# Kernel tuning notes

Hardware: AMD Instinct MI355X
Metric: run time of the kernel (lower is better)

The kernel has to match this reference:

```python
import jax, jax.numpy as jnp
import numpy as np
import math

B, H, W, C = 8, 112, 112, 192
WS, SHIFT, NH = 7, 3, 6
HD = C // NH
N = WS * WS
NW = (H // WS) * (W // WS)
MLP_HID = 4 * C
LOG100 = math.log(100.0)


def _rel_table():
    ch = np.arange(-(WS - 1), WS, dtype=np.float32)
    t = np.stack(np.meshgrid(ch, ch, indexing='ij')).transpose(1, 2, 0).reshape(-1, 2)
    t = t / float(WS - 1) * 8.0
    t = np.sign(t) * np.log2(np.abs(t) + 1.0) / np.log2(8.0)
    return t.astype(np.float32)  # ((2*WS-1)^2, 2)


def _rel_index():
    coords = np.stack(np.meshgrid(np.arange(WS), np.arange(WS), indexing='ij')).reshape(2, -1)
    rel = (coords[:, :, None] - coords[:, None, :]).transpose(1, 2, 0)
    rel = rel + np.array([WS - 1, WS - 1])
    rel = rel * np.array([2 * WS - 1, 1])
    return rel.sum(-1).astype(np.int32)  # (N, N)


def _attn_mask():
    img = np.zeros((H, W), dtype=np.float32)
    cnt = 0
    for hsl in (slice(0, -WS), slice(-WS, -SHIFT), slice(-SHIFT, None)):
        for wsl in (slice(0, -WS), slice(-WS, -SHIFT), slice(-SHIFT, None)):
            img[hsl, wsl] = cnt
            cnt += 1
    mw = img.reshape(H // WS, WS, W // WS, WS).transpose(0, 2, 1, 3).reshape(-1, N)
    diff = mw[:, None, :] - mw[:, :, None]
    return np.where(diff != 0, -100.0, 0.0).astype(np.float32)  # (NW, N, N)

REL_TABLE = jnp.asarray(_rel_table())
REL_INDEX = jnp.asarray(_rel_index())
ATTN_MASK = jnp.asarray(_attn_mask())


def _ln(v, g, b, eps=1e-5):
    m = jnp.mean(v, axis=-1, keepdims=True)
    s = jnp.mean((v - m) ** 2, axis=-1, keepdims=True)
    return (v - m) / jnp.sqrt(s + eps) * g + b


def setup_inputs() -> dict:
    key = jax.random.key(0)
    ks = jax.random.split(key, 12)
    std = 0.02
    inp = {
        'x': jax.random.normal(ks[0], (B, H * W, C), jnp.float32),
        'q_w': jax.random.normal(ks[1], (C, C), jnp.float32) * std,
        'q_b': jnp.zeros((C,), jnp.float32),
        'k_w': jax.random.normal(ks[2], (C, C), jnp.float32) * std,
        'v_w': jax.random.normal(ks[3], (C, C), jnp.float32) * std,
        'v_b': jnp.zeros((C,), jnp.float32),
        'proj_w': jax.random.normal(ks[4], (C, C), jnp.float32) * std,
        'proj_b': jnp.zeros((C,), jnp.float32),
        'logit_scale': jnp.log(10.0 * jnp.ones((NH, 1, 1), jnp.float32)),
        'cpb_w0': jax.random.normal(ks[5], (2, 512), jnp.float32) * std,
        'cpb_b0': jnp.zeros((512,), jnp.float32),
        'cpb_w1': jax.random.normal(ks[6], (512, NH), jnp.float32) * std,
        'ln1_g': jnp.ones((C,), jnp.float32),
        'ln1_b': jnp.zeros((C,), jnp.float32),
        'ln2_g': jnp.ones((C,), jnp.float32),
        'ln2_b': jnp.zeros((C,), jnp.float32),
        'fc1_w': jax.random.normal(ks[7], (C, MLP_HID), jnp.float32) * std,
        'fc1_b': jnp.zeros((MLP_HID,), jnp.float32),
        'fc2_w': jax.random.normal(ks[8], (MLP_HID, C), jnp.float32) * std,
        'fc2_b': jnp.zeros((C,), jnp.float32),
    }
    return inp


def reference(x, q_w, q_b, k_w, v_w, v_b, proj_w, proj_b, logit_scale,
              cpb_w0, cpb_b0, cpb_w1, ln1_g, ln1_b, ln2_g, ln2_b,
              fc1_w, fc1_b, fc2_w, fc2_b):
    shortcut = x  # (B, L, C)
    h = x.reshape(B, H, W, C)
    # cyclic shift
    h = jnp.roll(h, shift=(-SHIFT, -SHIFT), axis=(1, 2))
    # window partition -> (B*NW, N, C)
    h = h.reshape(B, H // WS, WS, W // WS, WS, C).transpose(0, 1, 3, 2, 4, 5)
    h = h.reshape(B * NW, N, C)

    q = (h @ q_w + q_b).reshape(-1, N, NH, HD).transpose(0, 2, 1, 3)
    k = (h @ k_w).reshape(-1, N, NH, HD).transpose(0, 2, 1, 3)
    v = (h @ v_w + v_b).reshape(-1, N, NH, HD).transpose(0, 2, 1, 3)

    # cosine-similarity attention
    q = q / jnp.maximum(jnp.linalg.norm(q, axis=-1, keepdims=True), 1e-6)
    k = k / jnp.maximum(jnp.linalg.norm(k, axis=-1, keepdims=True), 1e-6)
    scale = jnp.exp(jnp.minimum(logit_scale, LOG100))  # (NH,1,1)
    attn = jnp.einsum('bhqd,bhkd->bhqk', q, k) * scale

    # relative position bias via CPB MLP
    rpb = jax.nn.relu(REL_TABLE @ cpb_w0 + cpb_b0) @ cpb_w1  # (169, NH)
    rpb = rpb[REL_INDEX.reshape(-1)].reshape(N, N, NH).transpose(2, 0, 1)
    rpb = 16.0 * jax.nn.sigmoid(rpb)  # (NH, N, N)
    attn = attn + rpb[None]

    # shift mask
    attn = attn.reshape(B, NW, NH, N, N) + ATTN_MASK[None, :, None]
    attn = attn.reshape(B * NW, NH, N, N)
    attn = jax.nn.softmax(attn, axis=-1)

    out = jnp.einsum('bhqk,bhkd->bhqd', attn, v)
    out = out.transpose(0, 2, 1, 3).reshape(B * NW, N, C)
    out = out @ proj_w + proj_b

    # window reverse + reverse shift
    out = out.reshape(B, H // WS, W // WS, WS, WS, C).transpose(0, 1, 3, 2, 4, 5)
    out = out.reshape(B, H, W, C)
    out = jnp.roll(out, shift=(SHIFT, SHIFT), axis=(1, 2)).reshape(B, H * W, C)

    # post-norm residual (Swin-v2)
    h1 = shortcut + _ln(out, ln1_g, ln1_b)
    mlp = jax.nn.gelu(h1 @ fc1_w + fc1_b) @ fc2_w + fc2_b
    return h1 + _ln(mlp, ln2_g, ln2_b)
```

## Files before the change

### kernel.cpp

```cpp
#include <hip/hip_runtime.h>

typedef unsigned short u16;
typedef unsigned int   u32;
typedef __attribute__((ext_vector_type(8))) short bf16x8;
typedef __attribute__((ext_vector_type(4))) float f32x4;

#define B_      8
#define HW_     112
#define C_      192
#define NH_     6
#define HD_     32
#define L_      (HW_*HW_)
#define M_      (B_*L_)
#define MLP_    768
#define QKVN_   576
#define LOG100_ 4.6051702f
#define LOG2E_  1.44269504f

__device__ __forceinline__ float bf2f(u16 u){
  union { float f; u32 i; } v; v.i = ((u32)u) << 16; return v.f;
}
__device__ __forceinline__ u16 f2bf(float f){
  union { float f; u32 i; } v; v.f = f;
  u32 r = (v.i + 0x7fffu + ((v.i >> 16) & 1u)) >> 16;
  return (u16)r;
}
__device__ __forceinline__ u32 pk2(float a, float b){
  return (u32)f2bf(a) | ((u32)f2bf(b) << 16);
}
__device__ __forceinline__ u32 cvtpk(float a, float b){
  u32 r;
  asm volatile("v_cvt_pk_bf16_f32 %0, %1, %2" : "=v"(r) : "v"(a), "v"(b));
  return r;
}
__device__ __forceinline__ void u4_to_f8(uint4 u, float* f){
  f[0]=bf2f((u16)(u.x&0xffffu)); f[1]=bf2f((u16)(u.x>>16));
  f[2]=bf2f((u16)(u.y&0xffffu)); f[3]=bf2f((u16)(u.y>>16));
  f[4]=bf2f((u16)(u.z&0xffffu)); f[5]=bf2f((u16)(u.z>>16));
  f[6]=bf2f((u16)(u.w&0xffffu)); f[7]=bf2f((u16)(u.w>>16));
}

__device__ __forceinline__ int rowelem(int b, int wh, int ww, int t){
  int i = t/7, j = t - i*7;
  int oi = wh*7 + i + 3; if (oi >= 112) oi -= 112;
  int oj = ww*7 + j + 3; if (oj >= 112) oj -= 112;
  return b*L_ + oi*112 + oj;
}

__global__ __launch_bounds__(256) void prep_weights(
    const float* __restrict__ qw, const float* __restrict__ qb,
    const float* __restrict__ kw, const float* __restrict__ vw,
    const float* __restrict__ vb, const float* __restrict__ pw,
    const float* __restrict__ pb, const float* __restrict__ f1w,
    const float* __restrict__ f1b, const float* __restrict__ f2w,
    const float* __restrict__ f2b,
    u16* __restrict__ wt_qkv, float* __restrict__ b_qkv,
    u16* __restrict__ wt_p,   float* __restrict__ b_p,
    u16* __restrict__ wt_f1,  float* __restrict__ b_f1,
    u16* __restrict__ wt_f2,  float* __restrict__ b_f2)
{
  const int S1 = 110592, S2 = 147456, S3 = 294912, S4 = 442368, TOT = 444096;
  int i = blockIdx.x*256 + threadIdx.x;
  if (i >= TOT) return;
  if (i < S1) {
    int n = i/192, k = i%192;
    float v = (n<192) ? qw[k*192+n] : ((n<384) ? kw[k*192+(n-192)] : vw[k*192+(n-384)]);
    wt_qkv[i] = f2bf(v);
  } else if (i < S2) {
    int j = i - S1; int n = j/192, k = j%192;
    wt_p[j] = f2bf(pw[k*192+n]);
  } else if (i < S3) {
    int j = i - S2; int n = j/192, k = j%192;
    wt_f1[j] = f2bf(f1w[k*768+n]);
  } else if (i < S4) {
    int j = i - S3; int n = j/768, k = j%768;
    wt_f2[j] = f2bf(f2w[k*192+n]);
  } else {
    int j = i - S4;
    if (j < 576)        b_qkv[j] = (j<192) ? qb[j] : ((j<384) ? 0.f : vb[j-384]);
    else if (j < 768)   b_p[j-576]   = pb[j-576];
    else if (j < 1536)  b_f1[j-768]  = f1b[j-768];
    else                b_f2[j-1536] = f2b[j-1536];
  }
}

__device__ __forceinline__ float reltab(float x){
  float v = x * (8.f/6.f);
  float r = __log2f(fabsf(v) + 1.f) * (1.f/3.f);
  return (v < 0.f) ? -r : r;
}

__global__ __launch_bounds__(64) void rpb_a_kernel(
    const float* __restrict__ w0, const float* __restrict__ b0,
    const float* __restrict__ w1, float* __restrict__ rpb169)
{
  int tt = blockIdx.x, lane = threadIdx.x;
  float t0 = reltab((float)(tt/13 - 6));
  float t1 = reltab((float)(tt%13 - 6));
  float acc[6] = {0.f,0.f,0.f,0.f,0.f,0.f};
  for (int j = lane; j < 512; j += 64){
    float hid = fmaxf(t0*w0[j] + t1*w0[512+j] + b0[j], 0.f);
#pragma unroll
    for (int h=0; h<6; h++) acc[h] += hid * w1[j*6+h];
  }
#pragma unroll
  for (int h=0; h<6; h++){
#pragma unroll
    for (int m=32; m>=1; m>>=1) acc[h] += __shfl_xor(acc[h], m);
  }
  if (lane == 0){
#pragma unroll
    for (int h=0; h<6; h++) rpb169[tt*6+h] = acc[h];
  }
}

__global__ __launch_bounds__(256) void rpb_b_kernel(
    const float* __restrict__ rpb169, float* __restrict__ biasQ)
{
  int i = blockIdx.x*256 + threadIdx.x;
  if (i >= 98304) return;
  int key = i & 63, q = (i >> 6) & 63;
  int rest = i >> 12;
  int hh = rest % 6, type = rest / 6;
  float val;
  if (key >= 49) val = -60000.f;
  else if (q >= 49) val = 0.f;
  else {
    int qi = q/7, qj = q%7, ki = key/7, kj = key%7;
    int idx = (qi - ki + 6)*13 + (qj - kj + 6);
    float x = rpb169[idx*6 + hh];
    float sig = 16.f / (1.f + __expf(-x));
    int th = type >> 1, tw = type & 1;
    int rq = (th ? (qi<4?1:2) : 0)*3 + (tw ? (qj<4?1:2) : 0);
    int rk = (th ? (ki<4?1:2) : 0)*3 + (tw ? (kj<4?1:2) : 0);
    float msk = (rq != rk) ? -100.f : 0.f;
    val = (sig + msk) * LOG2E_;
  }
  biasQ[i] = val;
}

__device__ __forceinline__ float fast_gelu(float v){
  float t = v*v;
  float w = v * fmaf(-0.1029432f, t, -2.30220817f);
  float e = exp2f(w);
  return v * __builtin_amdgcn_rcpf(1.f + e);
}

template<int K, bool GELU>
__global__ __launch_bounds__(512,4) void gemm_kernel(
    const u16* __restrict__ A, const u16* __restrict__ Wt,
    const float* __restrict__ bias, u16* __restrict__ out, int NN)
{
  __shared__ __align__(16) u16 lds[10240];
  const int tid  = threadIdx.x;
  const int wave = tid >> 6, lane = tid & 63;
  const int m0 = blockIdx.x * 128;
  const int n0 = blockIdx.y * 192;
  const int wr = wave >> 1, wc = wave & 1;
  const int lrow = lane >> 2, lslot = lane & 3;
  const int gk = (lslot ^ ((lrow >> 1) & 3)) * 8;

  const u16* gsrc[3]; u32 ldst[3]; int nst = (wave < 4) ? 3 : 2;
#pragma unroll
  for (int t=0; t<3; t++){
    int c = wave + t*8;
    if (c < 8)       { gsrc[t] = A  + (size_t)(m0 + c*16 + lrow)*K + gk;      ldst[t] = c*512; }
    else if (c < 20) { gsrc[t] = Wt + (size_t)(n0 + (c-8)*16 + lrow)*K + gk;  ldst[t] = 4096 + (c-8)*512; }
  }
  const int lr16 = lane & 15;
  const int slot8 = ((lane >> 4) ^ ((lr16 >> 1) & 3)) * 8;
  u32 aoff[2], boff[6];
#pragma unroll
  for (int mt=0; mt<2; mt++) aoff[mt] = (u32)((wr*32 + mt*16 + lr16)*32 + slot8);
#pragma unroll
  for (int nt=0; nt<6; nt++) boff[nt] = (u32)(4096 + (wc*96 + nt*16 + lr16)*32 + slot8);

  float bs[6];
#pragma unroll
  for (int nt=0; nt<6; nt++) bs[nt] = bias[n0 + wc*96 + nt*16 + lr16];

  f32x4 acc[2][6];
#pragma unroll
  for (int mt=0; mt<2; mt++)
#pragma unroll
    for (int nt=0; nt<6; nt++)
      acc[mt][nt] = (f32x4){0.f,0.f,0.f,0.f};

  for (int k0 = 0; k0 < K; k0 += 32) {
#pragma unroll
    for (int t=0; t<3; t++){
      if (t < nst) {
        __builtin_amdgcn_global_load_lds(
            (const __attribute__((address_space(1))) void*)gsrc[t],
            (__attribute__((address_space(3))) void*)&lds[ldst[t]], 16, 0, 0);
        gsrc[t] += 32;
      }
    }
    __syncthreads();
    bf16x8 af[2], bf[6];
#pragma unroll
    for (int mt=0; mt<2; mt++) af[mt] = *(const bf16x8*)&lds[aoff[mt]];
#pragma unroll
    for (int nt=0; nt<6; nt++) bf[nt] = *(const bf16x8*)&lds[boff[nt]];
#pragma unroll
    for (int mt=0; mt<2; mt++)
#pragma unroll
      for (int nt=0; nt<6; nt++)
        acc[mt][nt] = __builtin_amdgcn_mfma_f32_16x16x32_bf16(af[mt], bf[nt], acc[mt][nt], 0, 0, 0);
    __syncthreads();
  }
#pragma unroll
  for (int mt=0; mt<2; mt++){
    int rbase = m0 + wr*32 + mt*16 + (lane >> 4)*4;
#pragma unroll
    for (int nt=0; nt<6; nt++){
      int col = n0 + wc*96 + nt*16 + lr16;
#pragma unroll
      for (int r2=0; r2<4; r2++){
        float v = acc[mt][nt][r2] + bs[nt];
        if (GELU) v = fast_gelu(v);
        out[(size_t)(rbase + r2)*NN + col] = f2bf(v);
      }
    }
  }
}

__global__ __launch_bounds__(512,4) void gemm_qkv_kernel(
    const float* __restrict__ X, const u16* __restrict__ Wt,
    const float* __restrict__ bias, u16* __restrict__ out)
{
  __shared__ __align__(16) u16 lds[10240];
  const int tid  = threadIdx.x;
  const int wave = tid >> 6, lane = tid & 63;
  const int m0 = blockIdx.x * 128;
  const int n0 = blockIdx.y * 192;
  const int wr = wave >> 1, wc = wave & 1;
  const int lrow = lane >> 2, lslot = lane & 3;
  const int gk = (lslot ^ ((lrow >> 1) & 3)) * 8;

  const u16* gsrcB[2]; u32 ldstB[2]; int nstB = (wave < 4) ? 2 : 1;
#pragma unroll
  for (int t=0; t<2; t++){
    int c = wave + t*8;
    if (c < 12) { gsrcB[t] = Wt + (size_t)(n0 + c*16 + lrow)*192 + gk; ldstB[t] = 4096 + c*512; }
  }
  const int ar = tid >> 2, as = tid & 3;
  const float* gsrcA = X + (size_t)(m0 + ar)*192 + as*8;
  const u32 dsta = (u32)(ar*32 + (as ^ ((ar >> 1) & 3))*8);

  const int lr16 = lane & 15;
  const int slot8 = ((lane >> 4) ^ ((lr16 >> 1) & 3)) * 8;
  u32 aoff[2], boff[6];
#pragma unroll
  for (int mt=0; mt<2; mt++) aoff[mt] = (u32)((wr*32 + mt*16 + lr16)*32 + slot8);
#pragma unroll
  for (int nt=0; nt<6; nt++) boff[nt] = (u32)(4096 + (wc*96 + nt*16 + lr16)*32 + slot8);

  float bs[6];
#pragma unroll
  for (int nt=0; nt<6; nt++) bs[nt] = bias[n0 + wc*96 + nt*16 + lr16];

  f32x4 acc[2][6];
#pragma unroll
  for (int mt=0; mt<2; mt++)
#pragma unroll
    for (int nt=0; nt<6; nt++)
      acc[mt][nt] = (f32x4){0.f,0.f,0.f,0.f};

  for (int k0 = 0; k0 < 192; k0 += 32) {
#pragma unroll
    for (int t=0; t<2; t++){
      if (t < nstB) {
        __builtin_amdgcn_global_load_lds(
            (const __attribute__((address_space(1))) void*)gsrcB[t],
            (__attribute__((address_space(3))) void*)&lds[ldstB[t]], 16, 0, 0);
        gsrcB[t] += 32;
      }
    }
    float4 a0 = *(const float4*)gsrcA;
    float4 a1 = *(const float4*)(gsrcA + 4);
    gsrcA += 32;
    uint4 aw;
    aw.x = cvtpk(a0.y, a0.x); aw.x = pk2(a0.x, a0.y);
    aw.x = pk2(a0.x, a0.y); aw.y = pk2(a0.z, a0.w);
    aw.z = pk2(a1.x, a1.y); aw.w = pk2(a1.z, a1.w);
    *(uint4*)(void*)&lds[dsta] = aw;
    __syncthreads();
    bf16x8 af[2], bf[6];
#pragma unroll
    for (int mt=0; mt<2; mt++) af[mt] = *(const bf16x8*)&lds[aoff[mt]];
#pragma unroll
    for (int nt=0; nt<6; nt++) bf[nt] = *(const bf16x8*)&lds[boff[nt]];
#pragma unroll
    for (int mt=0; mt<2; mt++)
#pragma unroll
      for (int nt=0; nt<6; nt++)
        acc[mt][nt] = __builtin_amdgcn_mfma_f32_16x16x32_bf16(af[mt], bf[nt], acc[mt][nt], 0, 0, 0);
    __syncthreads();
  }
#pragma unroll
  for (int mt=0; mt<2; mt++){
    int rbase = m0 + wr*32 + mt*16 + (lane >> 4)*4;
#pragma unroll
    for (int nt=0; nt<6; nt++){
      int col = n0 + wc*96 + nt*16 + lr16;
#pragma unroll
      for (int r2=0; r2<4; r2++){
        float v = acc[mt][nt][r2] + bs[nt];
        out[(size_t)(rbase + r2)*QKVN_ + col] = f2bf(v);
      }
    }
  }
}

__global__ __launch_bounds__(64) void attn_kernel(
    const u16* __restrict__ qkv, const float* __restrict__ lsc,
    const float* __restrict__ biasQ, u16* __restrict__ attn_out)
{
  __shared__ __align__(16) u16 smem[6144];
  char* smb = (char*)smem;
  const int id = blockIdx.x;
  const int hh = id % 6;
  const int w  = id / 6;
  const int b  = w >> 8;
  const int wh = (w >> 4) & 15, ww = w & 15;
  const int lane = threadIdx.x;
  const int lg = lane >> 4, lr = lane & 15;
  const int type = ((wh==15)?2:0) + ((ww==15)?1:0);
  const float qscale = __expf(fminf(lsc[hh], LOG100_)) * LOG2E_;

  union BU { bf16x8 v; u32 u[4]; };

  const int myrow = rowelem(b, wh, ww, min(lane, 48));

  {
    const u16* vsrc = qkv + (size_t)myrow*QKVN_ + 384 + hh*32;
#pragma unroll
    for (int r=0; r<4; r++){
      uint4 u = *(const uint4*)(vsrc + r*8);
      u32 wds[4] = {u.x, u.y, u.z, u.w};
#pragma unroll
      for (int i=0; i<8; i++){
        int d = r*8 + i;
        u16 val = (u16)(wds[i>>1] >> ((i&1)*16));
        int addr = 8192 + ((d*128 + lane*2) ^ ((d&7)<<4));
        *(u16*)(smb + addr) = val;
      }
    }
  }

  int rowq[4];
#pragma unroll
  for (int t=0; t<4; t++) rowq[t] = __shfl(myrow, t*16 + lr);

  bf16x8 qf[4], kf[4];
#pragma unroll
  for (int qt=0; qt<4; qt++){
    const u16* base = qkv + (size_t)rowq[qt]*QKVN_ + hh*32 + lg*8;
    uint4 u = *(const uint4*)base;
    float f[8]; u4_to_f8(u, f);
    float ss = 0.f;
#pragma unroll
    for (int d=0; d<8; d++) ss += f[d]*f[d];
    ss += __shfl_xor(ss, 16); ss += __shfl_xor(ss, 32);
    float rn = qscale * __builtin_amdgcn_rcpf(fmaxf(sqrtf(ss), 1e-6f));
    BU bu;
#pragma unroll
    for (int p=0; p<4; p++) bu.u[p] = cvtpk(f[2*p]*rn, f[2*p+1]*rn);
    qf[qt] = bu.v;
  }
#pragma unroll
  for (int kt=0; kt<4; kt++){
    const u16* base = qkv + (size_t)rowq[kt]*QKVN_ + 192 + hh*32 + lg*8;
    uint4 u = *(const uint4*)base;
    float f[8]; u4_to_f8(u, f);
    float ss = 0.f;
#pragma unroll
    for (int d=0; d<8; d++) ss += f[d]*f[d];
    ss += __shfl_xor(ss, 16); ss += __shfl_xor(ss, 32);
    float rn = __builtin_amdgcn_rcpf(fmaxf(sqrtf(ss), 1e-6f));
    BU bu;
#pragma unroll
    for (int p=0; p<4; p++) bu.u[p] = cvtpk(f[2*p]*rn, f[2*p+1]*rn);
    kf[kt] = bu.v;
  }

  f32x4 s2[4][4];
#pragma unroll
  for (int kt=0; kt<4; kt++)
#pragma unroll
    for (int qt=0; qt<4; qt++)
      s2[kt][qt] = __builtin_amdgcn_mfma_f32_16x16x32_bf16(kf[kt], qf[qt],
                     (f32x4){0.f,0.f,0.f,0.f}, 0, 0, 0);

  const float* bq = biasQ + (size_t)(type*6 + hh)*4096;
#pragma unroll
  for (int qt=0; qt<4; qt++){
    int q = qt*16 + lr;
#pragma unroll
    for (int kt=0; kt<4; kt++){
      f32x4 bv = *(const f32x4*)(bq + q*64 + kt*16 + lg*4);
      s2[kt][qt] += bv;
    }
  }

#pragma unroll
  for (int qt=0; qt<4; qt++){
    float m = s2[0][qt][0];
#pragma unroll
    for (int kt=0; kt<4; kt++)
#pragma unroll
      for (int r2=0; r2<4; r2++) m = fmaxf(m, s2[kt][qt][r2]);
    m = fmaxf(m, __shfl_xor(m, 16));
    m = fmaxf(m, __shfl_xor(m, 32));
    float sum = 0.f;
#pragma unroll
    for (int kt=0; kt<4; kt++)
#pragma unroll
      for (int r2=0; r2<4; r2++){
        float e = exp2f(s2[kt][qt][r2] - m);
        s2[kt][qt][r2] = e; sum += e;
      }
    sum += __shfl_xor(sum, 16);
    sum += __shfl_xor(sum, 32);
    float rs = __builtin_amdgcn_rcpf(sum);
#pragma unroll
    for (int kt=0; kt<4; kt++)
#pragma unroll
      for (int r2=0; r2<4; r2++) s2[kt][qt][r2] *= rs;
  }

#pragma unroll
  for (int qt=0; qt<4; qt++){
    int q = qt*16 + lr;
    int rowb = q*128, swz = (q&7)<<4;
#pragma unroll
    for (int kt=0; kt<4; kt++){
      u32 lo = cvtpk(s2[kt][qt][0], s2[kt][qt][1]);
      u32 hi = cvtpk(s2[kt][qt][2], s2[kt][qt][3]);
      int addr = (rowb + kt*32 + lg*8) ^ swz;
      *(uint2*)(smb + addr) = make_uint2(lo, hi);
    }
  }
  __syncthreads();

  f32x4 o[4][2];
#pragma unroll
  for (int mt=0; mt<4; mt++)
#pragma unroll
    for (int dt=0; dt<2; dt++)
      o[mt][dt] = (f32x4){0.f,0.f,0.f,0.f};

#pragma unroll
  for (int kb=0; kb<2; kb++){
    bf16x8 pf[4];
#pragma unroll
    for (int mt=0; mt<4; mt++){
      int q = mt*16 + lr;
      int addr = (q*128 + kb*64 + lg*16) ^ ((q&7)<<4);
      pf[mt] = *(const bf16x8*)(smb + addr);
    }
    bf16x8 vf[2];
#pragma unroll
    for (int dt=0; dt<2; dt++){
      int d = lr + dt*16;
      int addr = 8192 + ((d*128 + kb*64 + lg*16) ^ ((d&7)<<4));
      vf[dt] = *(const bf16x8*)(smb + addr);
    }
#pragma unroll
    for (int mt=0; mt<4; mt++)
#pragma unroll
      for (int dt=0; dt<2; dt++)
        o[mt][dt] = __builtin_amdgcn_mfma_f32_16x16x32_bf16(pf[mt], vf[dt], o[mt][dt], 0, 0, 0);
  }
  __syncthreads();

#pragma unroll
  for (int mt=0; mt<4; mt++)
#pragma unroll
    for (int r2=0; r2<4; r2++){
      int q = mt*16 + lg*4 + r2;
      int swz = (q&7)<<4;
#pragma unroll
      for (int dt=0; dt<2; dt++){
        int d = lr + dt*16;
        int addr = (q*128 + d*4) ^ swz;
        *(float*)(smb + addr) = o[mt][dt][r2];
      }
    }
  __syncthreads();
  if (lane < 49){
    int q = lane;
    float vals[32];
#pragma unroll
    for (int c=0; c<8; c++){
      int addr = (q*128 + c*16) ^ ((q&7)<<4);
      f32x4 v4 = *(const f32x4*)(smb + addr);
      vals[c*4+0]=v4[0]; vals[c*4+1]=v4[1]; vals[c*4+2]=v4[2]; vals[c*4+3]=v4[3];
    }
    u16* op = attn_out + (size_t)myrow*C_ + hh*32;
#pragma unroll
    for (int j=0; j<4; j++){
      uint4 u;
      u.x = cvtpk(vals[j*8+0], vals[j*8+1]);
      u.y = cvtpk(vals[j*8+2], vals[j*8+3]);
      u.z = cvtpk(vals[j*8+4], vals[j*8+5]);
      u.w = cvtpk(vals[j*8+6], vals[j*8+7]);
      *(uint4*)(void*)(op + j*8) = u;
    }
  }
}

template<bool BASE32, bool OUT32>
__global__ __launch_bounds__(256) void ln_res_kernel(
    const float* __restrict__ base32, const u16* __restrict__ base16,
    const u16* __restrict__ y,
    const float* __restrict__ gg, const float* __restrict__ bb,
    float* __restrict__ out32, u16* __restrict__ out16)
{
  int row  = blockIdx.x*4 + (threadIdx.x >> 6);
  int lane = threadIdx.x & 63;
  size_t ro = (size_t)row*192;
  float v0 = bf2f(y[ro+lane]), v1 = bf2f(y[ro+lane+64]), v2 = bf2f(y[ro+lane+128]);
  float s  = v0+v1+v2;
  float sq = v0*v0+v1*v1+v2*v2;
#pragma unroll
  for (int m=32; m>=1; m>>=1){ s += __shfl_xor(s,m); sq += __shfl_xor(sq,m); }
  float mean = s*(1.f/192.f);
  float var  = fmaxf(sq*(1.f/192.f) - mean*mean, 0.f);
  float rstd = rsqrtf(var + 1e-5f);
  float g0=gg[lane], g1=gg[lane+64], g2=gg[lane+128];
  float b0=bb[lane], b1=bb[lane+64], b2=bb[lane+128];
  float a0, a1, a2;
  if (BASE32) { a0=base32[ro+lane]; a1=base32[ro+lane+64]; a2=base32[ro+lane+128]; }
  else        { a0=bf2f(base16[ro+lane]); a1=bf2f(base16[ro+lane+64]); a2=bf2f(base16[ro+lane+128]); }
  float r0 = a0 + (v0-mean)*rstd*g0 + b0;
  float r1 = a1 + (v1-mean)*rstd*g1 + b1;
  float r2 = a2 + (v2-mean)*rstd*g2 + b2;
  if (OUT32) {
    out32[ro+lane] = r0; out32[ro+lane+64] = r1; out32[ro+lane+128] = r2;
  } else {
    out16[ro+lane] = f2bf(r0); out16[ro+lane+64] = f2bf(r1); out16[ro+lane+128] = f2bf(r2);
  }
}

extern "C" void kernel_launch(void* const* d_in, const int* in_sizes, int n_in,
                              void* d_out, int out_size, void* d_ws, size_t ws_size,
                              hipStream_t stream)
{
  (void)in_sizes; (void)n_in; (void)out_size; (void)ws_size;
  const float* x      = (const float*)d_in[0];
  const float* q_w    = (const float*)d_in[1];
  const float* q_b    = (const float*)d_in[2];
  const float* k_w    = (const float*)d_in[3];
  const float* v_w    = (const float*)d_in[4];
  const float* v_b    = (const float*)d_in[5];
  const float* proj_w = (const float*)d_in[6];
  const float* proj_b = (const float*)d_in[7];
  const float* lsc    = (const float*)d_in[8];
  const float* cpb_w0 = (const float*)d_in[9];
  const float* cpb_b0 = (const float*)d_in[10];
  const float* cpb_w1 = (const float*)d_in[11];
  const float* ln1_g  = (const float*)d_in[12];
  const float* ln1_b  = (const float*)d_in[13];
  const float* ln2_g  = (const float*)d_in[14];
  const float* ln2_b  = (const float*)d_in[15];
  const float* fc1_w  = (const float*)d_in[16];
  const float* fc1_b  = (const float*)d_in[17];
  const float* fc2_w  = (const float*)d_in[18];
  const float* fc2_b  = (const float*)d_in[19];

  char* ws = (char*)d_ws;
  size_t o = 0;
  u16* qkvb = (u16*)(ws + o);
  u16* mid  = qkvb;              o += 154140672;
  u16* attn_o = (u16*)(ws + o);
  u16* h1b    = attn_o;          o += 38535168;
  u16* proj_o = (u16*)(ws + o);
  u16* m2     = proj_o;          o += 38535168;
  u16* wt_qkv = (u16*)(ws + o);  o += 221184;
  float* b_qkv= (float*)(ws + o);o += 2304;
  u16* wt_p   = (u16*)(ws + o);  o += 73728;
  float* b_p  = (float*)(ws + o);o += 768;
  u16* wt_f1  = (u16*)(ws + o);  o += 294912;
  float* b_f1 = (float*)(ws + o);o += 3072;
  u16* wt_f2  = (u16*)(ws + o);  o += 294912;
  float* b_f2 = (float*)(ws + o);o += 768;
  float* rpb169 = (float*)(ws + o); o += 4096;
  float* biasQ  = (float*)(ws + o); o += 393216;

  prep_weights<<<1735, 256, 0, stream>>>(q_w, q_b, k_w, v_w, v_b, proj_w, proj_b,
      fc1_w, fc1_b, fc2_w, fc2_b, wt_qkv, b_qkv, wt_p, b_p, wt_f1, b_f1, wt_f2, b_f2);
  rpb_a_kernel<<<169, 64, 0, stream>>>(cpb_w0, cpb_b0, cpb_w1, rpb169);
  rpb_b_kernel<<<384, 256, 0, stream>>>(rpb169, biasQ);

  gemm_qkv_kernel<<<dim3(784,3), 512, 0, stream>>>(x, wt_qkv, b_qkv, qkvb);
  attn_kernel<<<12288, 64, 0, stream>>>(qkvb, lsc, biasQ, attn_o);
  gemm_kernel<192,false><<<dim3(784,1), 512, 0, stream>>>(attn_o, wt_p, b_p, proj_o, 192);
  ln_res_kernel<true,false><<<25088, 256, 0, stream>>>(x, nullptr, proj_o,
      ln1_g, ln1_b, nullptr, h1b);
  gemm_kernel<192,true><<<dim3(784,4), 512, 0, stream>>>(h1b, wt_f1, b_f1, mid, 768);
  gemm_kernel<768,false><<<dim3(784,1), 512, 0, stream>>>(mid, wt_f2, b_f2, m2, 192);
  ln_res_kernel<false,true><<<25088, 256, 0, stream>>>(nullptr, h1b, m2,
      ln2_g, ln2_b, (float*)d_out, nullptr);
}
```

Measured before the change: 368.8 us.

## Fuse LayerNorm-residual into projection/FC2 GEMM epilogues and double-buffer GEMM LDS

Folds both post-norm LayerNorm+residual steps into the epilogues of the proj and fc2 GEMMs. The row statistics are reduced across waves through shared memory. This removes two standalone LN kernels and the round trip of the bf16 intermediate through memory. It also double-buffers the LDS tiles in all GEMMs so the next K-slice is prefetched while the current one runs through MFMA, and the QKV kernel converts with the packed bf16 convert instruction. Doubling LDS per block may lower occupancy.

Result: faster. 335.9 us (-8.9%).

```diff
diff --git a/kernel.cpp b/kernel.cpp
--- a/kernel.cpp
+++ b/kernel.cpp
@@ -30,7 +30,7 @@
 }
 __device__ __forceinline__ u32 cvtpk(float a, float b){
   u32 r;
-  asm volatile("v_cvt_pk_bf16_f32 %0, %1, %2" : "=v"(r) : "v"(a), "v"(b));
+  asm("v_cvt_pk_bf16_f32 %0, %1, %2" : "=v"(r) : "v"(a), "v"(b));
   return r;
 }
 __device__ __forceinline__ void u4_to_f8(uint4 u, float* f){
@@ -139,6 +139,7 @@
   biasQ[i] = val;
 }
 
+
 __device__ __forceinline__ float fast_gelu(float v){
   float t = v*v;
   float w = v * fmaf(-0.1029432f, t, -2.30220817f);
@@ -146,12 +147,19 @@
   return v * __builtin_amdgcn_rcpf(1.f + e);
 }
 
-template<int K, bool GELU>
-__global__ __launch_bounds__(512,4) void gemm_kernel(
+#define MODE_GELU 0
+#define MODE_LN1  1
+#define MODE_LN2  2
+
+template<int K, int MODE>
+__global__ __launch_bounds__(512,4) void gemm_fused(
     const u16* __restrict__ A, const u16* __restrict__ Wt,
-    const float* __restrict__ bias, u16* __restrict__ out, int NN)
+    const float* __restrict__ bias,
+    const float* __restrict__ lng, const float* __restrict__ lnb,
+    const float* __restrict__ base32, const u16* __restrict__ base16,
+    u16* __restrict__ out16, float* __restrict__ out32, int NN)
 {
-  __shared__ __align__(16) u16 lds[10240];
+  __shared__ __align__(16) u16 lds[20480];
   const int tid  = threadIdx.x;
   const int wave = tid >> 6, lane = tid & 63;
   const int m0 = blockIdx.x * 128;
@@ -160,24 +168,22 @@
   const int lrow = lane >> 2, lslot = lane & 3;
   const int gk = (lslot ^ ((lrow >> 1) & 3)) * 8;
 
-  const u16* gsrc[3]; u32 ldst[3]; int nst = (wave < 4) ? 3 : 2;
+  const u16* gsrc[3]; u32 ldst[3]; const int nst = (wave < 4) ? 3 : 2;
 #pragma unroll
   for (int t=0; t<3; t++){
     int c = wave + t*8;
-    if (c < 8)       { gsrc[t] = A  + (size_t)(m0 + c*16 + lrow)*K + gk;      ldst[t] = c*512; }
-    else if (c < 20) { gsrc[t] = Wt + (size_t)(n0 + (c-8)*16 + lrow)*K + gk;  ldst[t] = 4096 + (c-8)*512; }
+    if (c < 8)       { gsrc[t] = A  + (size_t)(m0 + c*16 + lrow)*K + gk;      ldst[t] = (u32)(c*512); }
+    else if (c < 20) { gsrc[t] = Wt + (size_t)(n0 + (c-8)*16 + lrow)*K + gk;  ldst[t] = (u32)(4096 + (c-8)*512); }
+    else             { gsrc[t] = A; ldst[t] = 0; }
   }
   const int lr16 = lane & 15;
-  const int slot8 = ((lane >> 4) ^ ((lr16 >> 1) & 3)) * 8;
+  const int lg   = lane >> 4;
+  const int slot8 = (lg ^ ((lr16 >> 1) & 3)) * 8;
   u32 aoff[2], boff[6];
 #pragma unroll
   for (int mt=0; mt<2; mt++) aoff[mt] = (u32)((wr*32 + mt*16 + lr16)*32 + slot8);
 #pragma unroll
   for (int nt=0; nt<6; nt++) boff[nt] = (u32)(4096 + (wc*96 + nt*16 + lr16)*32 + slot8);
-
-  float bs[6];
-#pragma unroll
-  for (int nt=0; nt<6; nt++) bs[nt] = bias[n0 + wc*96 + nt*16 + lr16];
 
   f32x4 acc[2][6];
 #pragma unroll
@@ -186,22 +192,29 @@
     for (int nt=0; nt<6; nt++)
       acc[mt][nt] = (f32x4){0.f,0.f,0.f,0.f};
 
-  for (int k0 = 0; k0 < K; k0 += 32) {
-#pragma unroll
-    for (int t=0; t<3; t++){
-      if (t < nst) {
+  const int NT = K/32;
+#pragma unroll
+  for (int s=0; s<3; s++) if (s < nst)
+    __builtin_amdgcn_global_load_lds(
+        (const __attribute__((address_space(1))) void*)gsrc[s],
+        (__attribute__((address_space(3))) void*)&lds[ldst[s]], 16, 0, 0);
+  __syncthreads();
+
+  for (int t=0; t<NT; t++){
+    const u32 pb = (u32)(t&1)*10240u;
+    if (t+1 < NT){
+      const u32 pn = pb ^ 10240u;
+#pragma unroll
+      for (int s=0; s<3; s++) if (s < nst)
         __builtin_amdgcn_global_load_lds(
-            (const __attribute__((address_space(1))) void*)gsrc[t],
-            (__attribute__((address_space(3))) void*)&lds[ldst[t]], 16, 0, 0);
-        gsrc[t] += 32;
-      }
-    }
-    __syncthreads();
+            (const __attribute__((address_space(1))) void*)(gsrc[s] + (t+1)*32),
+            (__attribute__((address_space(3))) void*)&lds[ldst[s] + pn], 16, 0, 0);
+    }
     bf16x8 af[2], bf[6];
 #pragma unroll
-    for (int mt=0; mt<2; mt++) af[mt] = *(const bf16x8*)&lds[aoff[mt]];
-#pragma unroll
-    for (int nt=0; nt<6; nt++) bf[nt] = *(const bf16x8*)&lds[boff[nt]];
+    for (int mt=0; mt<2; mt++) af[mt] = *(const bf16x8*)&lds[pb + aoff[mt]];
+#pragma unroll
+    for (int nt=0; nt<6; nt++) bf[nt] = *(const bf16x8*)&lds[pb + boff[nt]];
 #pragma unroll
     for (int mt=0; mt<2; mt++)
 #pragma unroll
@@ -209,17 +222,97 @@
         acc[mt][nt] = __builtin_amdgcn_mfma_f32_16x16x32_bf16(af[mt], bf[nt], acc[mt][nt], 0, 0, 0);
     __syncthreads();
   }
-#pragma unroll
-  for (int mt=0; mt<2; mt++){
-    int rbase = m0 + wr*32 + mt*16 + (lane >> 4)*4;
+
+#pragma unroll
+  for (int nt=0; nt<6; nt++){
+    float bsv = bias[n0 + wc*96 + nt*16 + lr16];
+#pragma unroll
+    for (int mt=0; mt<2; mt++)
+#pragma unroll
+      for (int r2=0; r2<4; r2++) acc[mt][nt][r2] += bsv;
+  }
+
+  if (MODE == MODE_GELU){
+#pragma unroll
+    for (int mt=0; mt<2; mt++){
+      int rbase = m0 + wr*32 + mt*16 + lg*4;
+#pragma unroll
+      for (int nt=0; nt<6; nt++){
+        int col = n0 + wc*96 + nt*16 + lr16;
+#pragma unroll
+        for (int r2=0; r2<4; r2++)
+          out16[(size_t)(rbase + r2)*NN + col] = f2bf(fast_gelu(acc[mt][nt][r2]));
+      }
+    }
+  } else {
+    float sv[2][4], sq[2][4];
+#pragma unroll
+    for (int mt=0; mt<2; mt++)
+#pragma unroll
+      for (int r2=0; r2<4; r2++){
+        float s=0.f, q=0.f;
+#pragma unroll
+        for (int nt=0; nt<6; nt++){ float x = acc[mt][nt][r2]; s += x; q += x*x; }
+        sv[mt][r2]=s; sq[mt][r2]=q;
+      }
+#pragma unroll
+    for (int d=1; d<16; d<<=1){
+#pragma unroll
+      for (int mt=0; mt<2; mt++)
+#pragma unroll
+        for (int r2=0; r2<4; r2++){
+          sv[mt][r2] += __shfl_xor(sv[mt][r2], d);
+          sq[mt][r2] += __shfl_xor(sq[mt][r2], d);
+        }
+    }
+    float* red = (float*)lds;
+    if (lr16 == 0){
+#pragma unroll
+      for (int mt=0; mt<2; mt++)
+#pragma unroll
+        for (int r2=0; r2<4; r2++){
+          int row = wr*32 + mt*16 + lg*4 + r2;
+          red[row*4 + wc*2]     = sv[mt][r2];
+          red[row*4 + wc*2 + 1] = sq[mt][r2];
+        }
+    }
+    __syncthreads();
+    float mean[2][4], rstd[2][4];
+#pragma unroll
+    for (int mt=0; mt<2; mt++)
+#pragma unroll
+      for (int r2=0; r2<4; r2++){
+        int row = wr*32 + mt*16 + lg*4 + r2;
+        float s = red[row*4] + red[row*4+2];
+        float q = red[row*4+1] + red[row*4+3];
+        float m = s*(1.f/192.f);
+        float v = fmaxf(q*(1.f/192.f) - m*m, 0.f);
+        mean[mt][r2] = m; rstd[mt][r2] = rsqrtf(v + 1e-5f);
+      }
+    float gg[6], be[6];
 #pragma unroll
     for (int nt=0; nt<6; nt++){
       int col = n0 + wc*96 + nt*16 + lr16;
-#pragma unroll
-      for (int r2=0; r2<4; r2++){
-        float v = acc[mt][nt][r2] + bs[nt];
-        if (GELU) v = fast_gelu(v);
-        out[(size_t)(rbase + r2)*NN + col] = f2bf(v);
+      gg[nt] = lng[col]; be[nt] = lnb[col];
+    }
+#pragma unroll
+    for (int mt=0; mt<2; mt++){
+      int rbase = m0 + wr*32 + mt*16 + lg*4;
+#pragma unroll
+      for (int nt=0; nt<6; nt++){
+        int col = n0 + wc*96 + nt*16 + lr16;
+#pragma unroll
+        for (int r2=0; r2<4; r2++){
+          size_t idx = (size_t)(rbase + r2)*192 + col;
+          float r = (acc[mt][nt][r2] - mean[mt][r2])*rstd[mt][r2]*gg[nt] + be[nt];
+          if (MODE == MODE_LN1){
+            r += base32[idx];
+            out16[idx] = f2bf(r);
+          } else {
+            r += bf2f(base16[idx]);
+            out32[idx] = r;
+          }
+        }
       }
     }
   }
@@ -229,7 +322,7 @@
     const float* __restrict__ X, const u16* __restrict__ Wt,
     const float* __restrict__ bias, u16* __restrict__ out)
 {
-  __shared__ __align__(16) u16 lds[10240];
+  __shared__ __align__(16) u16 lds[20480];
   const int tid  = threadIdx.x;
   const int wave = tid >> 6, lane = tid & 63;
   const int m0 = blockIdx.x * 128;
@@ -238,27 +331,25 @@
   const int lrow = lane >> 2, lslot = lane & 3;
   const int gk = (lslot ^ ((lrow >> 1) & 3)) * 8;
 
-  const u16* gsrcB[2]; u32 ldstB[2]; int nstB = (wave < 4) ? 2 : 1;
+  const u16* gsrcB[2]; u32 ldstB[2]; const int nstB = (wave < 4) ? 2 : 1;
 #pragma unroll
   for (int t=0; t<2; t++){
     int c = wave + t*8;
-    if (c < 12) { gsrcB[t] = Wt + (size_t)(n0 + c*16 + lrow)*192 + gk; ldstB[t] = 4096 + c*512; }
+    if (c < 12) { gsrcB[t] = Wt + (size_t)(n0 + c*16 + lrow)*192 + gk; ldstB[t] = (u32)(4096 + c*512); }
+    else        { gsrcB[t] = Wt; ldstB[t] = 0; }
   }
   const int ar = tid >> 2, as = tid & 3;
-  const float* gsrcA = X + (size_t)(m0 + ar)*192 + as*8;
+  const float* gA = X + (size_t)(m0 + ar)*192 + as*8;
   const u32 dsta = (u32)(ar*32 + (as ^ ((ar >> 1) & 3))*8);
 
   const int lr16 = lane & 15;
-  const int slot8 = ((lane >> 4) ^ ((lr16 >> 1) & 3)) * 8;
+  const int lg   = lane >> 4;
+  const int slot8 = (lg ^ ((lr16 >> 1) & 3)) * 8;
   u32 aoff[2], boff[6];
 #pragma unroll
   for (int mt=0; mt<2; mt++) aoff[mt] = (u32)((wr*32 + mt*16 + lr16)*32 + slot8);
 #pragma unroll
   for (int nt=0; nt<6; nt++) boff[nt] = (u32)(4096 + (wc*96 + nt*16 + lr16)*32 + slot8);
-
-  float bs[6];
-#pragma unroll
-  for (int nt=0; nt<6; nt++) bs[nt] = bias[n0 + wc*96 + nt*16 + lr16];
 
   f32x4 acc[2][6];
 #pragma unroll
@@ -267,48 +358,62 @@
     for (int nt=0; nt<6; nt++)
       acc[mt][nt] = (f32x4){0.f,0.f,0.f,0.f};
 
-  for (int k0 = 0; k0 < 192; k0 += 32) {
-#pragma unroll
-    for (int t=0; t<2; t++){
-      if (t < nstB) {
+  {
+    float4 a0 = *(const float4*)gA;
+    float4 a1 = *(const float4*)(gA + 4);
+#pragma unroll
+    for (int s=0; s<2; s++) if (s < nstB)
+      __builtin_amdgcn_global_load_lds(
+          (const __attribute__((address_space(1))) void*)gsrcB[s],
+          (__attribute__((address_space(3))) void*)&lds[ldstB[s]], 16, 0, 0);
+    uint4 aw;
+    aw.x = cvtpk(a0.x, a0.y); aw.y = cvtpk(a0.z, a0.w);
+    aw.z = cvtpk(a1.x, a1.y); aw.w = cvtpk(a1.z, a1.w);
+    *(uint4*)(void*)&lds[dsta] = aw;
+  }
+  __syncthreads();
+
+  for (int t=0; t<6; t++){
+    const u32 pb = (u32)(t&1)*10240u;
+    const u32 pn = pb ^ 10240u;
+    float4 a0, a1;
+    if (t < 5){
+      a0 = *(const float4*)(gA + (t+1)*32);
+      a1 = *(const float4*)(gA + (t+1)*32 + 4);
+#pragma unroll
+      for (int s=0; s<2; s++) if (s < nstB)
         __builtin_amdgcn_global_load_lds(
-            (const __attribute__((address_space(1))) void*)gsrcB[t],
-            (__attribute__((address_space(3))) void*)&lds[ldstB[t]], 16, 0, 0);
-        gsrcB[t] += 32;
-      }
-    }
-    float4 a0 = *(const float4*)gsrcA;
-    float4 a1 = *(const float4*)(gsrcA + 4);
-    gsrcA += 32;
-    uint4 aw;
-    aw.x = cvtpk(a0.y, a0.x); aw.x = pk2(a0.x, a0.y);
-    aw.x = pk2(a0.x, a0.y); aw.y = pk2(a0.z, a0.w);
-    aw.z = pk2(a1.x, a1.y); aw.w = pk2(a1.z, a1.w);
-    *(uint4*)(void*)&lds[dsta] = aw;
-    __syncthreads();
+            (const __attribute__((address_space(1))) void*)(gsrcB[s] + (t+1)*32),
+            (__attribute__((address_space(3))) void*)&lds[ldstB[s] + pn], 16, 0, 0);
+    }
     bf16x8 af[2], bf[6];
 #pragma unroll
-    for (int mt=0; mt<2; mt++) af[mt] = *(const bf16x8*)&lds[aoff[mt]];
-#pragma unroll
-    for (int nt=0; nt<6; nt++) bf[nt] = *(const bf16x8*)&lds[boff[nt]];
+    for (int mt=0; mt<2; mt++) af[mt] = *(const bf16x8*)&lds[pb + aoff[mt]];
+#pragma unroll
+    for (int nt=0; nt<6; nt++) bf[nt] = *(const bf16x8*)&lds[pb + boff[nt]];
 #pragma unroll
     for (int mt=0; mt<2; mt++)
 #pragma unroll
       for (int nt=0; nt<6; nt++)
         acc[mt][nt] = __builtin_amdgcn_mfma_f32_16x16x32_bf16(af[mt], bf[nt], acc[mt][nt], 0, 0, 0);
+    if (t < 5){
+      uint4 aw;
+      aw.x = cvtpk(a0.x, a0.y); aw.y = cvtpk(a0.z, a0.w);
+      aw.z = cvtpk(a1.x, a1.y); aw.w = cvtpk(a1.z, a1.w);
+      *(uint4*)(void*)&lds[pn + dsta] = aw;
+    }
     __syncthreads();
   }
 #pragma unroll
   for (int mt=0; mt<2; mt++){
-    int rbase = m0 + wr*32 + mt*16 + (lane >> 4)*4;
+    int rbase = m0 + wr*32 + mt*16 + lg*4;
 #pragma unroll
     for (int nt=0; nt<6; nt++){
       int col = n0 + wc*96 + nt*16 + lr16;
-#pragma unroll
-      for (int r2=0; r2<4; r2++){
-        float v = acc[mt][nt][r2] + bs[nt];
-        out[(size_t)(rbase + r2)*QKVN_ + col] = f2bf(v);
-      }
+      float bsv = bias[col];
+#pragma unroll
+      for (int r2=0; r2<4; r2++)
+        out[(size_t)(rbase + r2)*QKVN_ + col] = f2bf(acc[mt][nt][r2] + bsv);
     }
   }
 }
@@ -508,39 +613,6 @@
       u.w = cvtpk(vals[j*8+6], vals[j*8+7]);
       *(uint4*)(void*)(op + j*8) = u;
     }
-  }
-}
-
-template<bool BASE32, bool OUT32>
-__global__ __launch_bounds__(256) void ln_res_kernel(
-    const float* __restrict__ base32, const u16* __restrict__ base16,
-    const u16* __restrict__ y,
-    const float* __restrict__ gg, const float* __restrict__ bb,
-    float* __restrict__ out32, u16* __restrict__ out16)
-{
-  int row  = blockIdx.x*4 + (threadIdx.x >> 6);
-  int lane = threadIdx.x & 63;
-  size_t ro = (size_t)row*192;
-  float v0 = bf2f(y[ro+lane]), v1 = bf2f(y[ro+lane+64]), v2 = bf2f(y[ro+lane+128]);
-  float s  = v0+v1+v2;
-  float sq = v0*v0+v1*v1+v2*v2;
-#pragma unroll
-  for (int m=32; m>=1; m>>=1){ s += __shfl_xor(s,m); sq += __shfl_xor(sq,m); }
-  float mean = s*(1.f/192.f);
-  float var  = fmaxf(sq*(1.f/192.f) - mean*mean, 0.f);
-  float rstd = rsqrtf(var + 1e-5f);
-  float g0=gg[lane], g1=gg[lane+64], g2=gg[lane+128];
-  float b0=bb[lane], b1=bb[lane+64], b2=bb[lane+128];
-  float a0, a1, a2;
-  if (BASE32) { a0=base32[ro+lane]; a1=base32[ro+lane+64]; a2=base32[ro+lane+128]; }
-  else        { a0=bf2f(base16[ro+lane]); a1=bf2f(base16[ro+lane+64]); a2=bf2f(base16[ro+lane+128]); }
-  float r0 = a0 + (v0-mean)*rstd*g0 + b0;
-  float r1 = a1 + (v1-mean)*rstd*g1 + b1;
-  float r2 = a2 + (v2-mean)*rstd*g2 + b2;
-  if (OUT32) {
-    out32[ro+lane] = r0; out32[ro+lane+64] = r1; out32[ro+lane+128] = r2;
-  } else {
-    out16[ro+lane] = f2bf(r0); out16[ro+lane+64] = f2bf(r1); out16[ro+lane+128] = f2bf(r2);
   }
 }
 
@@ -576,8 +648,6 @@
   u16* mid  = qkvb;              o += 154140672;
   u16* attn_o = (u16*)(ws + o);
   u16* h1b    = attn_o;          o += 38535168;
-  u16* proj_o = (u16*)(ws + o);
-  u16* m2     = proj_o;          o += 38535168;
   u16* wt_qkv = (u16*)(ws + o);  o += 221184;
   float* b_qkv= (float*)(ws + o);o += 2304;
   u16* wt_p   = (u16*)(ws + o);  o += 73728;
@@ -596,11 +666,10 @@
 
   gemm_qkv_kernel<<<dim3(784,3), 512, 0, stream>>>(x, wt_qkv, b_qkv, qkvb);
   attn_kernel<<<12288, 64, 0, stream>>>(qkvb, lsc, biasQ, attn_o);
-  gemm_kernel<192,false><<<dim3(784,1), 512, 0, stream>>>(attn_o, wt_p, b_p, proj_o, 192);
-  ln_res_kernel<true,false><<<25088, 256, 0, stream>>>(x, nullptr, proj_o,
-      ln1_g, ln1_b, nullptr, h1b);
-  gemm_kernel<192,true><<<dim3(784,4), 512, 0, stream>>>(h1b, wt_f1, b_f1, mid, 768);
-  gemm_kernel<768,false><<<dim3(784,1), 512, 0, stream>>>(mid, wt_f2, b_f2, m2, 192);
-  ln_res_kernel<false,true><<<25088, 256, 0, stream>>>(nullptr, h1b, m2,
-      ln2_g, ln2_b, (float*)d_out, nullptr);
-}
+  gemm_fused<192, MODE_LN1><<<dim3(784,1), 512, 0, stream>>>(
+      attn_o, wt_p, b_p, ln1_g, ln1_b, x, nullptr, h1b, nullptr, 192);
+  gemm_fused<192, MODE_GELU><<<dim3(784,4), 512, 0, stream>>>(
+      h1b, wt_f1, b_f1, nullptr, nullptr, nullptr, nullptr, mid, nullptr, 768);
+  gemm_fused<768, MODE_LN2><<<dim3(784,1), 512, 0, stream>>>(
+      mid, wt_f2, b_f2, ln2_g, ln2_b, nullptr, h1b, nullptr, (float*)d_out, 192);
+}
```
